# Kernel tuning notes

Hardware: AMD Instinct MI355X
Metric: run time of the kernel (lower is better)

The kernel has to match this reference:

```python
import jax, jax.numpy as jnp
import numpy as np

B_, J_, D_, E_, N_, K_ = 32, 1024, 192, 384, 16, 3


def _dwconv(x, w, b):
    # x: (B,J,E), w: (E,1,K) depthwise, b: (E,)
    xc = jnp.transpose(x, (0, 2, 1))  # (B,E,J)
    pad = w.shape[2] // 2
    y = jax.lax.conv_general_dilated(
        xc, w, window_strides=(1,), padding=[(pad, pad)],
        feature_group_count=w.shape[0], dimension_numbers=('NCH', 'OIH', 'NCH'))
    return jnp.transpose(y + b[None, :, None], (0, 2, 1))  # (B,J,E)


def _scan_dir(x, cw, cb, WB, bB, WC, bC, WD, bD, A, Wi, bi, Wr, br):
    # One directional selective-SSM pass. x: (B,J,E); A: (N,) negative diag.
    xc = _dwconv(x, cw, cb)                       # (B,J,E)
    Bt = xc @ WB + bB                             # (B,J,N)
    Ct = xc @ WC + bC                             # (B,J,N)
    Dt = jax.nn.softplus(xc @ WD + bD)            # Delta, (B,J,N)
    A_bar = jnp.exp(Dt * A)                       # ZOH discretization
    B_bar = (A_bar - 1.0) / (A + 1e-6) * Bt
    u = xc @ Wi + bi                              # in_to_state, (B,J,N)
    Bu = B_bar * u

    def step(h, ab_bu):
        ab, bu = ab_bu
        h = ab * h + bu
        return h, h

    h0 = jnp.zeros((x.shape[0], A.shape[0]), x.dtype)
    _, hs = jax.lax.scan(step, h0, (jnp.swapaxes(A_bar, 0, 1), jnp.swapaxes(Bu, 0, 1)))
    hs = jnp.swapaxes(hs, 0, 1)                   # (B,J,N)
    return (hs * Ct) @ Wr + br                    # readout, (B,J,E)


def setup_inputs() -> dict:
    key = jax.random.key(0)
    ks = iter(jax.random.split(key, 40))

    def nrm(shape, scale=0.02):
        return jax.random.normal(next(ks), shape, jnp.float32) * scale

    inp = {
        'tokens': jax.random.normal(next(ks), (B_, J_, D_), jnp.float32),
        'norm_g': jnp.ones((D_,), jnp.float32),
        'norm_b': jnp.zeros((D_,), jnp.float32),
        'Wx': nrm((D_, E_)), 'bx': jnp.zeros((E_,), jnp.float32),
        'Wz': nrm((D_, E_)), 'bz': jnp.zeros((E_,), jnp.float32),
        'convf_w': nrm((E_, 1, K_), 0.1), 'convf_b': jnp.zeros((E_,), jnp.float32),
        'convb_w': nrm((E_, 1, K_), 0.1), 'convb_b': jnp.zeros((E_,), jnp.float32),
        'WBf': nrm((E_, N_)), 'bBf': jnp.zeros((N_,), jnp.float32),
        'WCf': nrm((E_, N_)), 'bCf': jnp.zeros((N_,), jnp.float32),
        'WDf': nrm((E_, N_)), 'bDf': jnp.zeros((N_,), jnp.float32),
        'WBb': nrm((E_, N_)), 'bBb': jnp.zeros((N_,), jnp.float32),
        'WCb': nrm((E_, N_)), 'bCb': jnp.zeros((N_,), jnp.float32),
        'WDb': nrm((E_, N_)), 'bDb': jnp.zeros((N_,), jnp.float32),
        'A_log': nrm((N_,), 0.5),
        'Wi': nrm((E_, N_)), 'bi': jnp.zeros((N_,), jnp.float32),
        'Wr': nrm((N_, E_)), 'br': jnp.zeros((E_,), jnp.float32),
        'Wo': nrm((E_, D_)), 'bo': jnp.zeros((D_,), jnp.float32),
    }
    return inp


def reference(tokens, norm_g, norm_b, Wx, bx, Wz, bz, convf_w, convf_b,
              convb_w, convb_b, WBf, bBf, WCf, bCf, WDf, bDf, WBb, bBb,
              WCb, bCb, WDb, bDb, A_log, Wi, bi, Wr, br, Wo, bo):
    # LayerNorm (biased variance, eps=1e-5, like torch)
    mu = jnp.mean(tokens, axis=-1, keepdims=True)
    var = jnp.mean(jnp.square(tokens - mu), axis=-1, keepdims=True)
    t = (tokens - mu) / jnp.sqrt(var + 1e-5) * norm_g + norm_b

    x = t @ Wx + bx
    z = t @ Wz + bz
    gate = jax.nn.sigmoid(jax.nn.silu(z))

    # A computed under no_grad in torch -> stop_gradient here
    A = jax.lax.stop_gradient(-jax.nn.softplus(A_log))

    y_f = _scan_dir(x, convf_w, convf_b, WBf, bBf, WCf, bCf, WDf, bDf, A, Wi, bi, Wr, br)
    y_b = jnp.flip(_scan_dir(jnp.flip(x, 1), convb_w, convb_b, WBb, bBb, WCb, bCb,
                             WDb, bDb, A, Wi, bi, Wr, br), 1)
    y = (y_f + y_b) * gate
    return tokens + y @ Wo + bo
```

## Files before the change

kernel.cpp:

```cpp
#include <hip/hip_runtime.h>
#include <math.h>


typedef __attribute__((ext_vector_type(8))) short short8;
typedef __attribute__((ext_vector_type(4))) float f32x4;

__device__ __forceinline__ unsigned short f2bf(float f){
  union { float f; unsigned u; } v; v.f = f;
  unsigned r = v.u + 0x7FFFu + ((v.u >> 16) & 1u);
  return (unsigned short)(r >> 16);
}
__device__ __forceinline__ float bf2f(unsigned short s){
  union { unsigned u; float f; } v; v.u = ((unsigned)s) << 16;
  return v.f;
}
__device__ __forceinline__ float softplusf(float x){
  return (x > 20.f) ? x : log1pf(expf(x));
}
__device__ __forceinline__ float softplus_fast(float x){
  return (x > 20.f) ? x : __logf(1.f + __expf(x));
}
__device__ __forceinline__ float sigf_fast(float x){
  return __builtin_amdgcn_rcpf(1.f + __expf(-x));
}

__global__ __launch_bounds__(256) void prep_kernel(
    const float* __restrict__ Wx, const float* __restrict__ Wz,
    const float* __restrict__ WBf, const float* __restrict__ WCf,
    const float* __restrict__ WDf, const float* __restrict__ WBb,
    const float* __restrict__ WCb, const float* __restrict__ WDb,
    const float* __restrict__ Wi, const float* __restrict__ Wr,
    const float* __restrict__ Wo,
    const float* __restrict__ bBf, const float* __restrict__ bCf,
    const float* __restrict__ bDf, const float* __restrict__ bBb,
    const float* __restrict__ bCb, const float* __restrict__ bDb,
    const float* __restrict__ bi,
    unsigned short* __restrict__ Wxz_t, unsigned short* __restrict__ W4f_t,
    unsigned short* __restrict__ W4b_t, unsigned short* __restrict__ Wrt2,
    unsigned short* __restrict__ Wot, float* __restrict__ b4f,
    float* __restrict__ b4b)
{
  int idx = blockIdx.x * 256 + threadIdx.x;
  if (idx < 147456){ int n = idx / 192, k = idx % 192;
    Wxz_t[idx] = f2bf(n < 384 ? Wx[k*384 + n] : Wz[k*384 + n - 384]); return; }
  idx -= 147456;
  if (idx < 24576){ int n = idx / 384, k = idx % 384;
    const float* W = (n<16)?WBf:(n<32)?WCf:(n<48)?WDf:Wi;
    W4f_t[idx] = f2bf(W[k*16 + (n&15)]); return; }
  idx -= 24576;
  if (idx < 24576){ int n = idx / 384, k = idx % 384;
    const float* W = (n<16)?WBb:(n<32)?WCb:(n<48)?WDb:Wi;
    W4b_t[idx] = f2bf(W[k*16 + (n&15)]); return; }
  idx -= 24576;
  if (idx < 12288){ int n = idx / 32, k = idx % 32;
    Wrt2[idx] = f2bf(Wr[(k&15)*384 + n]); return; }
  idx -= 12288;
  if (idx < 73728){ int n = idx / 384, k = idx % 384;
    Wot[idx] = f2bf(Wo[k*192 + n]); return; }
  idx -= 73728;
  if (idx < 64){
    const float* bsel = (idx<16)?bBf:(idx<32)?bCf:(idx<48)?bDf:bi;
    b4f[idx] = bsel[idx & 15]; return; }
  idx -= 64;
  if (idx < 64){
    const float* bsel = (idx<16)?bBb:(idx<32)?bCb:(idx<48)?bDb:bi;
    b4b[idx] = bsel[idx & 15]; return; }
}

__global__ __launch_bounds__(256) void ln_kernel(
    const float* __restrict__ tokens, const float* __restrict__ g,
    const float* __restrict__ nb, unsigned short* __restrict__ t_bf)
{
  __shared__ unsigned short s[32 * 200];
  const int t = threadIdx.x;
  const int row0 = blockIdx.x * 32;
  {
    const int r = t >> 3, l8 = t & 7;
    const float* tr = tokens + (long)(row0 + r) * 192;
    float v[24], sm = 0.f, sq = 0.f;
#pragma unroll
    for (int i = 0; i < 24; i++){ float x = tr[l8 + 8*i]; v[i] = x; sm += x; sq += x*x; }
#pragma unroll
    for (int m = 1; m < 8; m <<= 1){ sm += __shfl_xor(sm, m); sq += __shfl_xor(sq, m); }
    const float mu = sm * (1.f/192.f);
    const float rstd = rsqrtf(sq * (1.f/192.f) - mu*mu + 1e-5f);
#pragma unroll
    for (int i = 0; i < 24; i++){
      const int d = l8 + 8*i;
      s[r*200 + d] = f2bf((v[i] - mu)*rstd*g[d] + nb[d]);
    }
  }
  __syncthreads();
  {
#pragma unroll
    for (int i = 0; i < 3; i++){
      const int item = i*256 + t;
      const int row = item / 24, c8 = item % 24;
      *(short8*)&t_bf[(long)(row0 + row)*192 + c8*8] =
          *(const short8*)&s[row*200 + c8*8];
    }
  }
}

__global__ __launch_bounds__(256) void xz_gemm(
    const unsigned short* __restrict__ t_bf,
    const unsigned short* __restrict__ Wxz_t,
    const float* __restrict__ bx, const float* __restrict__ bz,
    unsigned short* __restrict__ x_bf, unsigned short* __restrict__ gate_bf)
{
  __shared__ unsigned short tl[64 * 200];
  const int t = threadIdx.x;
  const int ct = blockIdx.x % 6;
  const int rt = blockIdx.x / 6;
  const int row0 = rt * 64;

  {
#pragma unroll
    for (int i = 0; i < 6; i++){
      const int item = i*256 + t;
      const int row = item / 24, c8 = item % 24;
      *(short8*)&tl[row*200 + c8*8] =
          *(const short8*)&t_bf[(long)(row0 + row)*192 + c8*8];
    }
  }
  __syncthreads();

  const int lane = t & 63, w = t >> 6;
  const int l15 = lane & 15, q = lane >> 4;
  const int C0 = ct*128 + w*32;

  f32x4 acc[4][2];
#pragma unroll
  for (int m = 0; m < 4; m++)
#pragma unroll
    for (int nf = 0; nf < 2; nf++) acc[m][nf] = (f32x4){0.f,0.f,0.f,0.f};

  const unsigned short* wb = Wxz_t + (long)(C0 + l15)*192 + q*8;
#pragma unroll
  for (int ks = 0; ks < 6; ks++){
    const int k0 = ks * 32;
    short8 a0 = *(const short8*)&tl[(     l15)*200 + k0 + q*8];
    short8 a1 = *(const short8*)&tl[(16 + l15)*200 + k0 + q*8];
    short8 a2 = *(const short8*)&tl[(32 + l15)*200 + k0 + q*8];
    short8 a3 = *(const short8*)&tl[(48 + l15)*200 + k0 + q*8];
#pragma unroll
    for (int nf = 0; nf < 2; nf++){
      short8 bw = *(const short8*)&wb[nf*16*192 + k0];
      acc[0][nf] = __builtin_amdgcn_mfma_f32_16x16x32_bf16(a0, bw, acc[0][nf], 0, 0, 0);
      acc[1][nf] = __builtin_amdgcn_mfma_f32_16x16x32_bf16(a1, bw, acc[1][nf], 0, 0, 0);
      acc[2][nf] = __builtin_amdgcn_mfma_f32_16x16x32_bf16(a2, bw, acc[2][nf], 0, 0, 0);
      acc[3][nf] = __builtin_amdgcn_mfma_f32_16x16x32_bf16(a3, bw, acc[3][nf], 0, 0, 0);
    }
  }
  __syncthreads();

  unsigned short* stg = tl;
  const int isgate = (ct >= 3);
#pragma unroll
  for (int nf = 0; nf < 2; nf++){
    const int c = C0 + nf*16 + l15;
    const float bv = isgate ? bz[c - 384] : bx[c];
#pragma unroll
    for (int m = 0; m < 4; m++){
#pragma unroll
      for (int r = 0; r < 4; r++){
        float val = acc[m][nf][r] + bv;
        if (isgate){ const float si = val * sigf_fast(val); val = sigf_fast(si); }
        stg[(m*16 + q*4 + r)*136 + (w*32 + nf*16 + l15)] = f2bf(val);
      }
    }
  }
  __syncthreads();

  {
    unsigned short* outp = isgate ? gate_bf : x_bf;
    const int cb = isgate ? (ct*128 - 384) : (ct*128);
#pragma unroll
    for (int i = 0; i < 4; i++){
      const int item = i*256 + t;
      const int row = item / 16, c8 = item % 16;
      *(short8*)&outp[(long)(row0 + row)*384 + cb + c8*8] =
          *(const short8*)&stg[row*136 + c8*8];
    }
  }
}

__global__ __launch_bounds__(256) void proj_mfma(
    const unsigned short* __restrict__ x_bf,
    const float* __restrict__ cwf, const float* __restrict__ cbf,
    const float* __restrict__ cwb, const float* __restrict__ cbb,
    const unsigned short* __restrict__ W4f, const unsigned short* __restrict__ W4b,
    const float* __restrict__ b4f, const float* __restrict__ b4b,
    const float* __restrict__ A_log,
    float* __restrict__ Af, float* __restrict__ Buf, float* __restrict__ Ctf,
    float* __restrict__ Ab, float* __restrict__ Bub, float* __restrict__ Ctb)
{
  __shared__ unsigned short xc[64 * 392];
  float* trans = (float*)xc;
  const int t = threadIdx.x;
  const int dir = blockIdx.x >> 9;
  const int bid = blockIdx.x & 511;
  const int b  = bid >> 4;
  const int j0 = (bid & 15) * 64;
  const float* cw = dir ? cwb : cwf;
  const float* cb = dir ? cbb : cbf;
  const unsigned short* W4 = dir ? W4b : W4f;
  const float* b4 = dir ? b4b : b4f;
  float* Aout = dir ? Ab  : Af;
  float* Bout = dir ? Bub : Buf;
  float* Cout = dir ? Ctb : Ctf;

  {
    const long xrow = (long)b * 1024 * 384;
#pragma unroll
    for (int half = 0; half < 2; half++){
      short8 xmv[6], x0v[6], xpv[6];
#pragma unroll
      for (int i = 0; i < 6; i++){
        const int idx = (half*6 + i)*256 + t;
        const int r = idx / 48;
        const int e0 = (idx - r*48) * 8;
        const int jp = j0 + r;
        xmv[i] = (short8){0,0,0,0,0,0,0,0};
        xpv[i] = (short8){0,0,0,0,0,0,0,0};
        if (jp >= 1){
          const int js = dir ? 1024 - jp : jp - 1;
          xmv[i] = *(const short8*)&x_bf[xrow + (long)js*384 + e0];
        }
        {
          const int js = dir ? 1023 - jp : jp;
          x0v[i] = *(const short8*)&x_bf[xrow + (long)js*384 + e0];
        }
        if (jp <= 1022){
          const int js = dir ? 1022 - jp : jp + 1;
          xpv[i] = *(const short8*)&x_bf[xrow + (long)js*384 + e0];
        }
      }
#pragma unroll
      for (int i = 0; i < 6; i++){
        const int idx = (half*6 + i)*256 + t;
        const int r = idx / 48;
        const int e0 = (idx - r*48) * 8;
        float wv[24], cbv[8];
#pragma unroll
        for (int v = 0; v < 6; v++)
          *(float4*)&wv[v*4] = *(const float4*)&cw[e0*3 + v*4];
#pragma unroll
        for (int v = 0; v < 2; v++)
          *(float4*)&cbv[v*4] = *(const float4*)&cb[e0 + v*4];
        short8 o;
#pragma unroll
        for (int m = 0; m < 8; m++){
          const float acc = fmaf(wv[3*m],   bf2f((unsigned short)xmv[i][m]),
                            fmaf(wv[3*m+1], bf2f((unsigned short)x0v[i][m]),
                            fmaf(wv[3*m+2], bf2f((unsigned short)xpv[i][m]), cbv[m])));
          o[m] = (short)f2bf(acc);
        }
        *(short8*)&xc[r*392 + e0] = o;
      }
    }
  }
  __syncthreads();

  const int lane = t & 63, w = t >> 6;
  const int l15 = lane & 15, q = lane >> 4;
  f32x4 acc[4];
#pragma unroll
  for (int nf = 0; nf < 4; nf++) acc[nf] = (f32x4){0.f,0.f,0.f,0.f};
  const unsigned short* wb = W4 + (long)l15*384 + q*8;
#pragma unroll
  for (int ks = 0; ks < 12; ks++){
    const int k0 = ks * 32;
    short8 a = *(const short8*)&xc[(w*16 + l15)*392 + k0 + q*8];
#pragma unroll
    for (int nf = 0; nf < 4; nf++){
      short8 bw = *(const short8*)&wb[nf*16*384 + k0];
      acc[nf] = __builtin_amdgcn_mfma_f32_16x16x32_bf16(a, bw, acc[nf], 0, 0, 0);
    }
  }
  __syncthreads();

  {
    const int n = l15;
    const float Av = -softplusf(A_log[n]);
    const float bB = b4[n], bC = b4[16+n], bD = b4[32+n], bU = b4[48+n];
    const float rAv = __builtin_amdgcn_rcpf(Av + 1e-6f);
#pragma unroll
    for (int r = 0; r < 4; r++){
      const int row = w*16 + q*4 + r;
      const float Bt  = acc[0][r] + bB;
      const float Ctv = acc[1][r] + bC;
      const float dt  = softplus_fast(acc[2][r] + bD);
      const float u   = acc[3][r] + bU;
      const float ab  = __expf(dt * Av);
      const float bu  = (ab - 1.f) * rAv * Bt * u;
      trans[(0*16 + n)*66 + row] = ab;
      trans[(1*16 + n)*66 + row] = bu;
      trans[(2*16 + n)*66 + row] = Ctv;
    }
  }
  __syncthreads();

  {
    const int j = t & 63, n4 = t >> 6;
#pragma unroll
    for (int i = 0; i < 4; i++){
      const int n = n4*4 + i;
      const int jp = j0 + j;
      const long base = ((long)b*16 + n) * 1024;
      Aout[base + jp] = trans[(0*16 + n)*66 + j];
      Bout[base + jp] = trans[(1*16 + n)*66 + j];
      Cout[base + (dir ? 1023 - jp : jp)] = trans[(2*16 + n)*66 + j];
    }
  }
}

__global__ __launch_bounds__(256) void scan2_kernel(
    const float* __restrict__ Af, const float* __restrict__ Buf, float* __restrict__ hsf,
    const float* __restrict__ Ab, const float* __restrict__ Bub, float* __restrict__ hsb)
{
  __shared__ float sA[256], sB[256];
  const int sel = blockIdx.x >> 9;
  const long base = (long)(blockIdx.x & 511) * 1024;
  const float* Abar = sel ? Ab  : Af;
  const float* Bu   = sel ? Bub : Buf;
  float* hs         = sel ? hsb : hsf;
  const int t = threadIdx.x;
  const float4 a4 = *reinterpret_cast<const float4*>(&Abar[base + t*4]);
  const float4 b4 = *reinterpret_cast<const float4*>(&Bu[base + t*4]);
  float A = a4.x, Bc = b4.x;
  Bc = fmaf(a4.y, Bc, b4.y); A *= a4.y;
  Bc = fmaf(a4.z, Bc, b4.z); A *= a4.z;
  Bc = fmaf(a4.w, Bc, b4.w); A *= a4.w;
  sA[t] = A; sB[t] = Bc;
  __syncthreads();
  for (int off = 1; off < 256; off <<= 1){
    const float cA = sA[t], cB = sB[t];
    float pA = 1.f, pB = 0.f;
    if (t >= off){ pA = sA[t - off]; pB = sB[t - off]; }
    __syncthreads();
    sA[t] = pA * cA;
    sB[t] = fmaf(cA, pB, cB);
    __syncthreads();
  }
  float h = (t > 0) ? sB[t - 1] : 0.f;
  float4 o;
  h = fmaf(a4.x, h, b4.x); o.x = h;
  h = fmaf(a4.y, h, b4.y); o.y = h;
  h = fmaf(a4.z, h, b4.z); o.z = h;
  h = fmaf(a4.w, h, b4.w); o.w = h;
  *reinterpret_cast<float4*>(&hs[base + t*4]) = o;
}

__global__ __launch_bounds__(256) void final_mfma(
    const float* __restrict__ tokens, const unsigned short* __restrict__ gate_bf,
    const float* __restrict__ hsf, const float* __restrict__ Ctf,
    const float* __restrict__ hsb, const float* __restrict__ Ctb,
    const unsigned short* __restrict__ Wrt2, const float* __restrict__ br,
    const unsigned short* __restrict__ Wot, const float* __restrict__ bo,
    float* __restrict__ out)
{
  __shared__ unsigned short s2[16 * 36];
  __shared__ float stgf[16 * 200];
  unsigned short* yg = (unsigned short*)stgf;
  const int t = threadIdx.x;
  const int b  = blockIdx.x >> 6;
  const int j0 = (blockIdx.x & 63) * 16;

  {
#pragma unroll
    for (int i = 0; i < 2; i++){
      const int idx = i*256 + t;
      const int j = idx & 15, kk = idx >> 4;
      float val;
      if (kk < 16){
        const long p = ((long)b*16 + kk)*1024 + j0 + j;
        val = hsf[p] * Ctf[p];
      } else {
        const long basen = ((long)b*16 + (kk - 16)) * 1024;
        val = hsb[basen + 1023 - (j0 + j)] * Ctb[basen + j0 + j];
      }
      s2[j*36 + kk] = f2bf(val);
    }
  }
  __syncthreads();

  const int lane = t & 63, w = t >> 6;
  const int l15 = lane & 15, q = lane >> 4;

  {
    short8 a = *(const short8*)&s2[l15*36 + q*8];
    const unsigned short* wbp = Wrt2 + (long)l15*32 + q*8;
#pragma unroll
    for (int i = 0; i < 6; i++){
      const int nf = w*6 + i;
      short8 bw = *(const short8*)&wbp[nf*16*32];
      f32x4 acc = (f32x4){0.f,0.f,0.f,0.f};
      acc = __builtin_amdgcn_mfma_f32_16x16x32_bf16(a, bw, acc, 0, 0, 0);
      const int c = nf*16 + l15;
      const float brv = 2.f * br[c];
#pragma unroll
      for (int r = 0; r < 4; r++)
        yg[(q*4 + r)*388 + c] = f2bf(acc[r] + brv);
    }
  }
  __syncthreads();

  {
#pragma unroll
    for (int i = 0; i < 3; i++){
      const int item = i*256 + t;
      const int row = item / 48;
      const int cb  = (item % 48) * 8;
      short8 y8 = *(const short8*)&yg[row*388 + cb];
      short8 g8 = *(const short8*)&gate_bf[((long)b*1024 + j0 + row)*384 + cb];
      short8 o;
#pragma unroll
      for (int m = 0; m < 8; m++)
        o[m] = (short)f2bf(bf2f((unsigned short)y8[m]) * bf2f((unsigned short)g8[m]));
      *(short8*)&yg[row*388 + cb] = o;
    }
  }
  __syncthreads();

  f32x4 acc[3];
  {
#pragma unroll
    for (int i = 0; i < 3; i++) acc[i] = (f32x4){0.f,0.f,0.f,0.f};
    const unsigned short* wbp = Wot + (long)l15*384 + q*8;
#pragma unroll
    for (int ks = 0; ks < 12; ks++){
      const int k0 = ks * 32;
      short8 a = *(const short8*)&yg[l15*388 + k0 + q*8];
#pragma unroll
      for (int i = 0; i < 3; i++){
        const int nf = w*3 + i;
        short8 bw = *(const short8*)&wbp[(long)nf*16*384 + k0];
        acc[i] = __builtin_amdgcn_mfma_f32_16x16x32_bf16(a, bw, acc[i], 0, 0, 0);
      }
    }
  }
  __syncthreads();

  {
    const int gq = q ^ (q >> 1);
#pragma unroll
    for (int i = 0; i < 3; i++){
      const int nf = w*3 + i;
      const int c = nf*16 + l15;
      const float bv = bo[c];
      const int scol = ((nf + gq) % 12)*16 + l15;
#pragma unroll
      for (int r = 0; r < 4; r++)
        stgf[(q*4 + r)*200 + scol] = acc[i][r] + bv;
    }
  }
  __syncthreads();

  {
#pragma unroll
    for (int i = 0; i < 3; i++){
      const int item = i*256 + t;
      const int row = item / 48;
      const int c4  = (item % 48) * 4;
      const int qq = (row >> 2) & 3;
      const int gg = qq ^ (qq >> 1);
      const int nf = c4 / 16;
      const int scol = ((nf + gg) % 12)*16 + (c4 % 16);
      float4 v = *(const float4*)&stgf[row*200 + scol];
      const long R = (long)b*1024 + j0 + row;
      const float4 tk = *(const float4*)&tokens[R*192 + c4];
      v.x += tk.x; v.y += tk.y; v.z += tk.z; v.w += tk.w;
      *(float4*)&out[R*192 + c4] = v;
    }
  }
}

extern "C" void kernel_launch(void* const* d_in, const int* in_sizes, int n_in,
                              void* d_out, int out_size, void* d_ws, size_t ws_size,
                              hipStream_t stream)
{
  const float* tokens  = (const float*)d_in[0];
  const float* norm_g  = (const float*)d_in[1];
  const float* norm_b  = (const float*)d_in[2];
  const float* Wx      = (const float*)d_in[3];
  const float* bx      = (const float*)d_in[4];
  const float* Wz      = (const float*)d_in[5];
  const float* bz      = (const float*)d_in[6];
  const float* convf_w = (const float*)d_in[7];
  const float* convf_b = (const float*)d_in[8];
  const float* convb_w = (const float*)d_in[9];
  const float* convb_b = (const float*)d_in[10];
  const float* WBf     = (const float*)d_in[11];
  const float* bBf     = (const float*)d_in[12];
  const float* WCf     = (const float*)d_in[13];
  const float* bCf     = (const float*)d_in[14];
  const float* WDf     = (const float*)d_in[15];
  const float* bDf     = (const float*)d_in[16];
  const float* WBb     = (const float*)d_in[17];
  const float* bBb     = (const float*)d_in[18];
  const float* WCb     = (const float*)d_in[19];
  const float* bCb     = (const float*)d_in[20];
  const float* WDb     = (const float*)d_in[21];
  const float* bDb     = (const float*)d_in[22];
  const float* A_log   = (const float*)d_in[23];
  const float* Wi      = (const float*)d_in[24];
  const float* bi      = (const float*)d_in[25];
  const float* Wr      = (const float*)d_in[26];
  const float* br      = (const float*)d_in[27];
  const float* Wo      = (const float*)d_in[28];
  const float* bo      = (const float*)d_in[29];

  char* ws = (char*)d_ws;
  unsigned short* x_bf    = (unsigned short*)(ws + 0);
  unsigned short* gate_bf = (unsigned short*)(ws + 25165824);
  unsigned short* Wxz_t   = (unsigned short*)(ws + 50331648);
  unsigned short* W4f_t   = (unsigned short*)(ws + 50626560);
  unsigned short* W4b_t   = (unsigned short*)(ws + 50675712);
  unsigned short* Wrt2    = (unsigned short*)(ws + 50724864);
  unsigned short* Wot     = (unsigned short*)(ws + 50749440);
  float* b4f = (float*)(ws + 50896896);
  float* b4b = (float*)(ws + 50897152);
  float* Af  = (float*)(ws + 50897408);
  float* Buf = (float*)(ws + 52994560);
  float* Ctf = (float*)(ws + 55091712);
  float* hsf = (float*)(ws + 57188864);
  float* Ab  = (float*)(ws + 59286016);
  float* Bub = (float*)(ws + 61383168);
  float* Ctb = (float*)(ws + 63480320);
  float* hsb = (float*)(ws + 65577472);
  unsigned short* t_bf = (unsigned short*)(ws + 67674624);

  prep_kernel<<<1105, 256, 0, stream>>>(Wx, Wz, WBf, WCf, WDf, WBb, WCb, WDb,
                                        Wi, Wr, Wo, bBf, bCf, bDf, bBb, bCb, bDb, bi,
                                        Wxz_t, W4f_t, W4b_t, Wrt2, Wot, b4f, b4b);
  ln_kernel<<<1024, 256, 0, stream>>>(tokens, norm_g, norm_b, t_bf);
  xz_gemm<<<3072, 256, 0, stream>>>(t_bf, Wxz_t, bx, bz, x_bf, gate_bf);
  proj_mfma<<<1024, 256, 0, stream>>>(x_bf, convf_w, convf_b, convb_w, convb_b,
                                      W4f_t, W4b_t, b4f, b4b, A_log,
                                      Af, Buf, Ctf, Ab, Bub, Ctb);
  scan2_kernel<<<1024, 256, 0, stream>>>(Af, Buf, hsf, Ab, Bub, hsb);
  final_mfma<<<2048, 256, 0, stream>>>(tokens, gate_bf, hsf, Ctf, hsb, Ctb,
                                       Wrt2, br, Wot, bo, (float*)d_out);
}
```

Before: 143.8 us.

## Halve proj_mfma tile to 32 rows and split MFMA output columns across waves

```diff
diff --git a/kernel.cpp b/kernel.cpp
--- a/kernel.cpp
+++ b/kernel.cpp
@@ -195,13 +195,13 @@
     float* __restrict__ Af, float* __restrict__ Buf, float* __restrict__ Ctf,
     float* __restrict__ Ab, float* __restrict__ Bub, float* __restrict__ Ctb)
 {
-  __shared__ unsigned short xc[64 * 392];
-  float* trans = (float*)xc;
+  __shared__ unsigned short xc[32 * 392];
+  float* pj = (float*)xc;
   const int t = threadIdx.x;
-  const int dir = blockIdx.x >> 9;
-  const int bid = blockIdx.x & 511;
-  const int b  = bid >> 4;
-  const int j0 = (bid & 15) * 64;
+  const int dir = blockIdx.x >> 10;
+  const int bid = blockIdx.x & 1023;
+  const int b  = bid >> 5;
+  const int j0 = (bid & 31) * 32;
   const float* cw = dir ? cwb : cwf;
   const float* cb = dir ? cbb : cbf;
   const unsigned short* W4 = dir ? W4b : W4f;
@@ -213,67 +213,59 @@
   {
     const long xrow = (long)b * 1024 * 384;
 #pragma unroll
-    for (int half = 0; half < 2; half++){
-      short8 xmv[6], x0v[6], xpv[6];
-#pragma unroll
-      for (int i = 0; i < 6; i++){
-        const int idx = (half*6 + i)*256 + t;
-        const int r = idx / 48;
-        const int e0 = (idx - r*48) * 8;
-        const int jp = j0 + r;
-        xmv[i] = (short8){0,0,0,0,0,0,0,0};
-        xpv[i] = (short8){0,0,0,0,0,0,0,0};
-        if (jp >= 1){
-          const int js = dir ? 1024 - jp : jp - 1;
-          xmv[i] = *(const short8*)&x_bf[xrow + (long)js*384 + e0];
-        }
-        {
-          const int js = dir ? 1023 - jp : jp;
-          x0v[i] = *(const short8*)&x_bf[xrow + (long)js*384 + e0];
-        }
-        if (jp <= 1022){
-          const int js = dir ? 1022 - jp : jp + 1;
-          xpv[i] = *(const short8*)&x_bf[xrow + (long)js*384 + e0];
-        }
-      }
-#pragma unroll
-      for (int i = 0; i < 6; i++){
-        const int idx = (half*6 + i)*256 + t;
-        const int r = idx / 48;
-        const int e0 = (idx - r*48) * 8;
-        float wv[24], cbv[8];
-#pragma unroll
-        for (int v = 0; v < 6; v++)
-          *(float4*)&wv[v*4] = *(const float4*)&cw[e0*3 + v*4];
-#pragma unroll
-        for (int v = 0; v < 2; v++)
-          *(float4*)&cbv[v*4] = *(const float4*)&cb[e0 + v*4];
-        short8 o;
-#pragma unroll
-        for (int m = 0; m < 8; m++){
-          const float acc = fmaf(wv[3*m],   bf2f((unsigned short)xmv[i][m]),
-                            fmaf(wv[3*m+1], bf2f((unsigned short)x0v[i][m]),
-                            fmaf(wv[3*m+2], bf2f((unsigned short)xpv[i][m]), cbv[m])));
-          o[m] = (short)f2bf(acc);
-        }
-        *(short8*)&xc[r*392 + e0] = o;
-      }
+    for (int i = 0; i < 6; i++){
+      const int idx = i*256 + t;
+      const int r = idx / 48;
+      const int e0 = (idx - r*48) * 8;
+      const int jp = j0 + r;
+      short8 xm = (short8){0,0,0,0,0,0,0,0};
+      short8 xp = (short8){0,0,0,0,0,0,0,0};
+      if (jp >= 1){
+        const int js = dir ? 1024 - jp : jp - 1;
+        xm = *(const short8*)&x_bf[xrow + (long)js*384 + e0];
+      }
+      short8 x0;
+      {
+        const int js = dir ? 1023 - jp : jp;
+        x0 = *(const short8*)&x_bf[xrow + (long)js*384 + e0];
+      }
+      if (jp <= 1022){
+        const int js = dir ? 1022 - jp : jp + 1;
+        xp = *(const short8*)&x_bf[xrow + (long)js*384 + e0];
+      }
+      float wv[24], cbv[8];
+#pragma unroll
+      for (int v = 0; v < 6; v++)
+        *(float4*)&wv[v*4] = *(const float4*)&cw[e0*3 + v*4];
+#pragma unroll
+      for (int v = 0; v < 2; v++)
+        *(float4*)&cbv[v*4] = *(const float4*)&cb[e0 + v*4];
+      short8 o;
+#pragma unroll
+      for (int m = 0; m < 8; m++){
+        const float acc = fmaf(wv[3*m],   bf2f((unsigned short)xm[m]),
+                          fmaf(wv[3*m+1], bf2f((unsigned short)x0[m]),
+                          fmaf(wv[3*m+2], bf2f((unsigned short)xp[m]), cbv[m])));
+        o[m] = (short)f2bf(acc);
+      }
+      *(short8*)&xc[r*392 + e0] = o;
     }
   }
   __syncthreads();
 
   const int lane = t & 63, w = t >> 6;
   const int l15 = lane & 15, q = lane >> 4;
-  f32x4 acc[4];
-#pragma unroll
-  for (int nf = 0; nf < 4; nf++) acc[nf] = (f32x4){0.f,0.f,0.f,0.f};
-  const unsigned short* wb = W4 + (long)l15*384 + q*8;
+  const int rt = w & 1, ng = w >> 1;
+  f32x4 acc[2];
+#pragma unroll
+  for (int nf = 0; nf < 2; nf++) acc[nf] = (f32x4){0.f,0.f,0.f,0.f};
+  const unsigned short* wb = W4 + (long)(ng*32 + l15)*384 + q*8;
 #pragma unroll
   for (int ks = 0; ks < 12; ks++){
     const int k0 = ks * 32;
-    short8 a = *(const short8*)&xc[(w*16 + l15)*392 + k0 + q*8];
-#pragma unroll
-    for (int nf = 0; nf < 4; nf++){
+    short8 a = *(const short8*)&xc[(rt*16 + l15)*392 + k0 + q*8];
+#pragma unroll
+    for (int nf = 0; nf < 2; nf++){
       short8 bw = *(const short8*)&wb[nf*16*384 + k0];
       acc[nf] = __builtin_amdgcn_mfma_f32_16x16x32_bf16(a, bw, acc[nf], 0, 0, 0);
     }
@@ -281,36 +273,33 @@
   __syncthreads();
 
   {
-    const int n = l15;
-    const float Av = -softplusf(A_log[n]);
-    const float bB = b4[n], bC = b4[16+n], bD = b4[32+n], bU = b4[48+n];
-    const float rAv = __builtin_amdgcn_rcpf(Av + 1e-6f);
-#pragma unroll
-    for (int r = 0; r < 4; r++){
-      const int row = w*16 + q*4 + r;
-      const float Bt  = acc[0][r] + bB;
-      const float Ctv = acc[1][r] + bC;
-      const float dt  = softplus_fast(acc[2][r] + bD);
-      const float u   = acc[3][r] + bU;
+#pragma unroll
+    for (int nf = 0; nf < 2; nf++){
+      const int col = ng*32 + nf*16 + l15;
+#pragma unroll
+      for (int r = 0; r < 4; r++)
+        pj[col*34 + rt*16 + q*4 + r] = acc[nf][r];
+    }
+  }
+  __syncthreads();
+
+  {
+#pragma unroll
+    for (int i = 0; i < 2; i++){
+      const int idx = i*256 + t;
+      const int n = idx >> 5, j = idx & 31;
+      const float Bt  = pj[(     n)*34 + j] + b4[n];
+      const float Ctv = pj[(16 + n)*34 + j] + b4[16 + n];
+      const float dt  = softplus_fast(pj[(32 + n)*34 + j] + b4[32 + n]);
+      const float u   = pj[(48 + n)*34 + j] + b4[48 + n];
+      const float Av  = -softplusf(A_log[n]);
       const float ab  = __expf(dt * Av);
-      const float bu  = (ab - 1.f) * rAv * Bt * u;
-      trans[(0*16 + n)*66 + row] = ab;
-      trans[(1*16 + n)*66 + row] = bu;
-      trans[(2*16 + n)*66 + row] = Ctv;
-    }
-  }
-  __syncthreads();
-
-  {
-    const int j = t & 63, n4 = t >> 6;
-#pragma unroll
-    for (int i = 0; i < 4; i++){
-      const int n = n4*4 + i;
+      const float bu  = (ab - 1.f) * __builtin_amdgcn_rcpf(Av + 1e-6f) * Bt * u;
       const int jp = j0 + j;
       const long base = ((long)b*16 + n) * 1024;
-      Aout[base + jp] = trans[(0*16 + n)*66 + j];
-      Bout[base + jp] = trans[(1*16 + n)*66 + j];
-      Cout[base + (dir ? 1023 - jp : jp)] = trans[(2*16 + n)*66 + j];
+      Aout[base + jp] = ab;
+      Bout[base + jp] = bu;
+      Cout[base + (dir ? 1023 - jp : jp)] = Ctv;
     }
   }
 }
@@ -536,7 +525,7 @@
                                         Wxz_t, W4f_t, W4b_t, Wrt2, Wot, b4f, b4b);
   ln_kernel<<<1024, 256, 0, stream>>>(tokens, norm_g, norm_b, t_bf);
   xz_gemm<<<3072, 256, 0, stream>>>(t_bf, Wxz_t, bx, bz, x_bf, gate_bf);
-  proj_mfma<<<1024, 256, 0, stream>>>(x_bf, convf_w, convf_b, convb_w, convb_b,
+  proj_mfma<<<2048, 256, 0, stream>>>(x_bf, convf_w, convf_b, convb_w, convb_b,
                                       W4f_t, W4b_t, b4f, b4b, A_log,
                                       Af, Buf, Ctf, Ab, Bub, Ctb);
   scan2_kernel<<<1024, 256, 0, stream>>>(Af, Buf, hsf, Ab, Bub, hsb);
```

After: 139.1 us. 1.03x faster.
